# Optimization experiments

Measured on AMD Instinct MI355X. Metric: run time of the kernel, lower is better.

The kernel has to match this reference:

```python
import jax, jax.numpy as jnp
import numpy as np

H_DIM = 1024
HEAD_DIM = 128
N_HEADS = 8
HD = HEAD_DIM * N_HEADS  # 1024


def setup_inputs() -> dict:
    key = jax.random.key(0)
    ks = jax.random.split(key, 32)
    B, S = 16, 1024
    inp = {
        "f_in": jax.random.normal(ks[0], (B, S, H_DIM), jnp.float32),
        "i_in": jax.random.normal(ks[1], (B, S, H_DIM), jnp.float32),
        "z_in": jax.random.normal(ks[2], (B, S, H_DIM), jnp.float32),
        "o_in": jax.random.normal(ks[3], (B, S, H_DIM), jnp.float32),
        "c0": jax.random.normal(ks[4], (B, N_HEADS, HEAD_DIM), jnp.float32),
        "h0": jax.random.normal(ks[5], (B, N_HEADS, HEAD_DIM), jnp.float32),
    }
    # Parameters (torch Linear stored here as [in, out]; init std=0.02, zero bias)
    names_x = ["Fx", "Ix", "Zx", "Ox"]
    names_h = ["Fh", "Ih", "Zh", "Oh"]
    for j, n in enumerate(names_x):
        inp[f"W_{n}"] = 0.02 * jax.random.normal(ks[6 + j], (H_DIM, HD), jnp.float32)
        inp[f"b_{n}"] = jnp.zeros((HD,), jnp.float32)
    for j, n in enumerate(names_h):
        inp[f"W_{n}"] = 0.02 * jax.random.normal(ks[10 + j], (HD, HD), jnp.float32)
        inp[f"b_{n}"] = jnp.zeros((HD,), jnp.float32)
    inp["W_post"] = 0.02 * jax.random.normal(ks[14], (HD, H_DIM), jnp.float32)
    inp["b_post"] = jnp.zeros((H_DIM,), jnp.float32)
    return inp


def reference(f_in, i_in, z_in, o_in, c0, h0,
              W_Fx, b_Fx, W_Ix, b_Ix, W_Zx, b_Zx, W_Ox, b_Ox,
              W_Fh, b_Fh, W_Ih, b_Ih, W_Zh, b_Zh, W_Oh, b_Oh,
              W_post, b_post):
    B, S, _ = f_in.shape
    # Precompute input-to-gate projections for all timesteps: (B,S,HD)
    fx = f_in @ W_Fx + b_Fx
    ix = i_in @ W_Ix + b_Ix
    zx = z_in @ W_Zx + b_Zx
    ox = o_in @ W_Ox + b_Ox
    # Flatten head state: gating is elementwise, heads are contiguous in HD
    c = c0.reshape(B, HD)
    h = h0.reshape(B, HD)
    # Time-major for scan: (S,B,HD)
    xs = (fx.transpose(1, 0, 2), ix.transpose(1, 0, 2),
          zx.transpose(1, 0, 2), ox.transpose(1, 0, 2))

    def step(carry, x):
        c, h = carry
        fx_t, ix_t, zx_t, ox_t = x
        f = jax.nn.sigmoid(fx_t + h @ W_Fh + b_Fh)
        i = jax.nn.sigmoid(ix_t + h @ W_Ih + b_Ih)
        z = jnp.tanh(zx_t + h @ W_Zh + b_Zh)
        o = jax.nn.sigmoid(ox_t + h @ W_Oh + b_Oh)
        c = f * c + i * z
        h = o * jnp.tanh(c)
        return (c, h), h

    (c, h), ys = jax.lax.scan(step, (c, h), xs)
    y = ys.transpose(1, 0, 2)  # (B,S,HD)
    y = y @ W_post + b_post    # n_heads > 1 -> post-head projection
    state = (c.reshape(B, N_HEADS, HEAD_DIM), h.reshape(B, N_HEADS, HEAD_DIM))
    return (y, state)
```

## Files before the change

### kernel.cpp

```cpp
#include <hip/hip_runtime.h>
#include <stdint.h>
#include <stddef.h>

typedef __attribute__((ext_vector_type(8))) short short8;
typedef __attribute__((ext_vector_type(4))) short short4_t;
typedef __attribute__((ext_vector_type(8))) unsigned short ushort8_t;
typedef __attribute__((ext_vector_type(4))) unsigned short ushort4_t;
typedef __attribute__((ext_vector_type(4))) float f32x4;
typedef __attribute__((ext_vector_type(4))) unsigned uint4_t;
typedef __attribute__((ext_vector_type(2))) unsigned uint2_t;

#define XG_BYTES  (134217728ull)
#define HS_BYTES  (33587200ull)
#define PAD_OFF   (XG_BYTES + HS_BYTES)
#define WT_OFF    (PAD_OFF + 32768ull)

#define SENT 0x7FC07FC0u

__device__ __forceinline__ unsigned short f2b(float f){
  unsigned u = __builtin_bit_cast(unsigned, f);
  u += 0x7fffu + ((u >> 16) & 1u);
  return (unsigned short)(u >> 16);
}
__device__ __forceinline__ float b2f(unsigned short b){
  unsigned u = ((unsigned)b) << 16;
  return __builtin_bit_cast(float, u);
}
__device__ __forceinline__ float sigm(float x){ return 1.0f / (1.0f + __expf(-x)); }
__device__ __forceinline__ float tanh_(float x){ return 2.0f / (1.0f + __expf(-2.0f*x)) - 1.0f; }

__device__ __forceinline__ void ld_h8_plain(const unsigned short* p, short8* a){
  asm volatile(
    "global_load_dwordx4 %0, %8, off\n\t"
    "global_load_dwordx4 %1, %8, off offset:64\n\t"
    "global_load_dwordx4 %2, %8, off offset:128\n\t"
    "global_load_dwordx4 %3, %8, off offset:192\n\t"
    "global_load_dwordx4 %4, %8, off offset:256\n\t"
    "global_load_dwordx4 %5, %8, off offset:320\n\t"
    "global_load_dwordx4 %6, %8, off offset:384\n\t"
    "global_load_dwordx4 %7, %8, off offset:448\n\t"
    "s_waitcnt vmcnt(0)"
    : "=&v"(a[0]), "=&v"(a[1]), "=&v"(a[2]), "=&v"(a[3]),
      "=&v"(a[4]), "=&v"(a[5]), "=&v"(a[6]), "=&v"(a[7])
    : "v"(p) : "memory");
}
__device__ __forceinline__ void st_u32_mall(unsigned* p, unsigned v){
  asm volatile("global_store_dword %0, %1, off sc0 sc1"
               :: "v"(p), "v"(v) : "memory");
}

__global__ __launch_bounds__(256) void k_prep(
    const float* __restrict__ w0, const float* __restrict__ w1,
    const float* __restrict__ w2, const float* __restrict__ w3,
    const float* __restrict__ w4, const float* __restrict__ w5,
    const float* __restrict__ w6, const float* __restrict__ w7,
    const float* __restrict__ w8, unsigned short* __restrict__ wt)
{
  const int z = blockIdx.z;
  const float* W = (z==0)?w0:(z==1)?w1:(z==2)?w2:(z==3)?w3:(z==4)?w4:
                   (z==5)?w5:(z==6)?w6:(z==7)?w7:w8;
  unsigned short* out = wt + (size_t)z*1024*1024;
  __shared__ float tile[64][65];
  const int k0 = blockIdx.x*64, n0 = blockIdx.y*64;
  const int tid = threadIdx.x;
  {
    const int kk = tid >> 2, nn0 = (tid & 3) * 16;
    const float* src = W + (size_t)(k0+kk)*1024 + n0 + nn0;
    #pragma unroll
    for (int j=0;j<16;j+=4){
      f32x4 v = *(const f32x4*)(src + j);
      tile[kk][nn0+j+0]=v[0]; tile[kk][nn0+j+1]=v[1];
      tile[kk][nn0+j+2]=v[2]; tile[kk][nn0+j+3]=v[3];
    }
  }
  __syncthreads();
  {
    const int nn = tid >> 2, kk0 = (tid & 3) * 16;
    ushort8_t a, b;
    #pragma unroll
    for (int j=0;j<8;++j){ a[j]=f2b(tile[kk0+j][nn]); b[j]=f2b(tile[kk0+8+j][nn]); }
    unsigned short* dst = out + (size_t)(n0+nn)*1024 + k0 + kk0;
    *(ushort8_t*)dst = a;
    *(ushort8_t*)(dst+8) = b;
  }
}

__global__ void k_init(const float* __restrict__ h0, unsigned short* __restrict__ hs){
  const int i = blockIdx.x*256 + threadIdx.x;
  unsigned v = (unsigned)f2b(h0[i]);
  asm volatile("global_store_short %0, %1, off sc0 sc1"
               :: "v"(hs + i), "v"(v) : "memory");
}

__global__ void k_fill(unsigned* __restrict__ xgw, unsigned* __restrict__ hsw){
  const size_t i = (size_t)blockIdx.x*256 + threadIdx.x;
  uint4_t v = (uint4_t){SENT, SENT, SENT, SENT};
  if (i < 8388608ull){
    asm volatile("global_store_dwordx4 %0, %1, off sc0 sc1"
                 :: "v"(xgw + i*4), "v"(v) : "memory");
  } else {
    asm volatile("global_store_dwordx4 %0, %1, off sc0 sc1"
                 :: "v"(hsw + 8192 + (i - 8388608ull)*4), "v"(v) : "memory");
  }
}

__global__ __launch_bounds__(256,1) void k_mega(
    const float* __restrict__ xF, const float* __restrict__ xI,
    const float* __restrict__ xZ, const float* __restrict__ xO,
    const float* __restrict__ bF, const float* __restrict__ bI,
    const float* __restrict__ bZ, const float* __restrict__ bO,
    const unsigned short* __restrict__ wt,
    const float* __restrict__ bfh, const float* __restrict__ bih,
    const float* __restrict__ bzh, const float* __restrict__ boh,
    const float* __restrict__ c0,
    unsigned short* __restrict__ xg,
    unsigned short* __restrict__ hs,
    const float* __restrict__ bpost,
    float* __restrict__ y,
    float* __restrict__ oc, float* __restrict__ oh)
{
  __shared__ __align__(16) char smem[32768];
  const int tid  = threadIdx.x;
  const int lane = tid & 63, wv = tid >> 6;
  const int l15  = lane & 15, lg = lane >> 4;

  if (blockIdx.x < 64){
    typedef f32x4 PartT[4][4][64];
    PartT* part = (PartT*)smem;

    const unsigned short* WtR = wt + (size_t)5*1048576;
    const int wg = blockIdx.x;
    const int n  = wg*16 + l15;

    short8 wf[4][8];
    #pragma unroll
    for (int g=0; g<4; ++g){
      const unsigned short* wp = WtR + (size_t)g*1048576 + (size_t)n*1024 + wv*256 + lg*8;
      #pragma unroll
      for (int c=0; c<8; ++c)
        wf[g][c] = *(const short8*)(wp + c*32);
    }

    float cst[4]; float bias[4];
    bias[0]=bfh[n]; bias[1]=bih[n]; bias[2]=bzh[n]; bias[3]=boh[n];
    #pragma unroll
    for (int r=0;r<4;++r) cst[r] = c0[(size_t)(lg*4+r)*1024 + n];

    unsigned* hsw = (unsigned*)hs;
    const int koff = l15*1024 + wv*256 + lg*8;

    float hv = 0.f;
    for (int t=0; t<1024; ++t){
      short4_t xq[4];
      {
        const unsigned short* xb = xg + (size_t)((t*4)*1024 + n)*16 + lg*4;
        asm volatile(
          "global_load_dwordx2 %0, %4, off\n\t"
          "global_load_dwordx2 %1, %5, off\n\t"
          "global_load_dwordx2 %2, %6, off\n\t"
          "global_load_dwordx2 %3, %7, off"
          : "=&v"(xq[0]), "=&v"(xq[1]), "=&v"(xq[2]), "=&v"(xq[3])
          : "v"(xb), "v"(xb + 16384), "v"(xb + 32768), "v"(xb + 49152)
          : "memory");
      }

      const unsigned short* hp = hs + (size_t)t*16384 + koff;
      short8 a[8];
      ld_h8_plain(hp, a);
      {
        bool bad[8]; bool any = false;
        #pragma unroll
        for (int c=0;c<8;++c){
          uint4_t q = __builtin_bit_cast(uint4_t, a[c]);
          bad[c] = (q[0]==SENT)||(q[1]==SENT)||(q[2]==SENT)||(q[3]==SENT);
          any = any | bad[c];
        }
        while (__any(any)){
          __builtin_amdgcn_s_sleep(1);
          #pragma unroll
          for (int c=0;c<8;++c)
            if (bad[c])
              asm volatile("global_load_dwordx4 %0, %1, off sc0 sc1"
                           : "+v"(a[c]) : "v"(hp + c*32) : "memory");
          asm volatile("s_waitcnt vmcnt(0)" ::: "memory");
          __builtin_amdgcn_sched_barrier(0);
          any = false;
          #pragma unroll
          for (int c=0;c<8;++c){
            uint4_t q = __builtin_bit_cast(uint4_t, a[c]);
            bad[c] = (q[0]==SENT)||(q[1]==SENT)||(q[2]==SENT)||(q[3]==SENT);
            any = any | bad[c];
          }
        }
      }
      {
        bool xb_[4]; bool anyx = false;
        #pragma unroll
        for (int g=0; g<4; ++g){
          uint2_t u = __builtin_bit_cast(uint2_t, xq[g]);
          xb_[g] = (u[0]==SENT)||(u[1]==SENT);
          anyx = anyx | xb_[g];
        }
        while (__any(anyx)){
          __builtin_amdgcn_s_sleep(2);
          const unsigned short* xb = xg + (size_t)((t*4)*1024 + n)*16 + lg*4;
          #pragma unroll
          for (int g=0; g<4; ++g)
            if (xb_[g])
              asm volatile("global_load_dwordx2 %0, %1, off sc0 sc1"
                           : "+v"(xq[g]) : "v"(xb + g*16384) : "memory");
          asm volatile("s_waitcnt vmcnt(0)" ::: "memory");
          __builtin_amdgcn_sched_barrier(0);
          anyx = false;
          #pragma unroll
          for (int g=0; g<4; ++g){
            uint2_t u = __builtin_bit_cast(uint2_t, xq[g]);
            xb_[g] = (u[0]==SENT)||(u[1]==SENT);
            anyx = anyx | xb_[g];
          }
        }
      }

      f32x4 acc[4];
      #pragma unroll
      for (int g=0;g<4;++g) acc[g] = (f32x4){0.f,0.f,0.f,0.f};
      #pragma unroll
      for (int c=0;c<8;++c){
        acc[0] = __builtin_amdgcn_mfma_f32_16x16x32_bf16(a[c], wf[0][c], acc[0], 0,0,0);
        acc[1] = __builtin_amdgcn_mfma_f32_16x16x32_bf16(a[c], wf[1][c], acc[1], 0,0,0);
        acc[2] = __builtin_amdgcn_mfma_f32_16x16x32_bf16(a[c], wf[2][c], acc[2], 0,0,0);
        acc[3] = __builtin_amdgcn_mfma_f32_16x16x32_bf16(a[c], wf[3][c], acc[3], 0,0,0);
      }
      const int pb = t & 1;
      #pragma unroll
      for (int g=0;g<4;++g) part[pb][wv][g][lane] = acc[g];
      __syncthreads();

      f32x4 r_[4];
      #pragma unroll
      for (int g=0;g<4;++g){
        f32x4 s0 = part[pb][0][g][lane];
        f32x4 s1 = part[pb][1][g][lane];
        f32x4 s2 = part[pb][2][g][lane];
        f32x4 s3 = part[pb][3][g][lane];
        r_[g] = (s0 + s1) + (s2 + s3);
      }

      float hvv[4];
      {
        const int r = wv;
        float pf = r_[0][r] + b2f((unsigned short)xq[0][r]) + bias[0];
        float pi = r_[1][r] + b2f((unsigned short)xq[1][r]) + bias[1];
        float pz = r_[2][r] + b2f((unsigned short)xq[2][r]) + bias[2];
        float po = r_[3][r] + b2f((unsigned short)xq[3][r]) + bias[3];
        float fg = sigm(pf), ig = sigm(pi), zg = tanh_(pz), og = sigm(po);
        float cn = fg*cst[r] + ig*zg;
        cst[r] = cn;
        hv = og * tanh_(cn);
        hvv[r] = hv;
        unsigned m  = (unsigned)f2b(hv);
        unsigned nb = (unsigned)__shfl_xor(m, 1);
        if ((l15 & 1) == 0){
          unsigned word = m | (nb << 16);
          unsigned* pw = hsw + (size_t)(t+1)*8192 + (size_t)(lg*4+wv)*512 + (n >> 1);
          st_u32_mall(pw, word);
        }
      }
      #pragma unroll
      for (int r=0;r<4;++r){
        if (r == wv) continue;
        float pf = r_[0][r] + b2f((unsigned short)xq[0][r]) + bias[0];
        float pi = r_[1][r] + b2f((unsigned short)xq[1][r]) + bias[1];
        float pz = r_[2][r] + b2f((unsigned short)xq[2][r]) + bias[2];
        float po = r_[3][r] + b2f((unsigned short)xq[3][r]) + bias[3];
        float fg = sigm(pf), ig = sigm(pi), zg = tanh_(pz), og = sigm(po);
        float cn = fg*cst[r] + ig*zg;
        cst[r] = cn;
        hvv[r] = og * tanh_(cn);
      }
      if (t == 1023 && wv == 0){
        #pragma unroll
        for (int r=0;r<4;++r){
          oc[(size_t)(lg*4+r)*1024 + n] = cst[r];
          oh[(size_t)(lg*4+r)*1024 + n] = hvv[r];
        }
      }
    }
    return;
  }

  unsigned short* AsmB = (unsigned short*)smem;
  unsigned short* BsmB = (unsigned short*)(smem + 8192);
  const int wid = blockIdx.x - 64;
  const int wy = wv >> 1, wx = wv & 1;
  const int rr = tid >> 1, kq = tid & 1;
  const int s0 = kq*2;
  unsigned short* aw0 = &AsmB[rr*32 + (((s0  ) ^ (rr&3))<<3)];
  unsigned short* aw1 = &AsmB[rr*32 + (((s0+1) ^ (rr&3))<<3)];
  unsigned short* bw0 = &BsmB[rr*32 + (((s0  ) ^ (rr&3))<<3)];
  unsigned short* bw1 = &BsmB[rr*32 + (((s0+1) ^ (rr&3))<<3)];

  for (int idx = wid; idx < 4096; idx += 192){
    const int tm = idx >> 5, rmn = idx & 31, tn = rmn >> 2, g = rmn & 3;
    const float* X  = (g==0)?xF:(g==1)?xI:(g==2)?xZ:xO;
    const float* Bp = (g==0)?bF:(g==1)?bI:(g==2)?bZ:bO;
    const unsigned short* Wg = wt + (size_t)g*1048576;

    const int ar = tm*128 + rr;
    const int ab = ar & 15, as_ = ar >> 4;
    const float* aptr = X + ((size_t)ab*1024 + as_)*1024 + kq*16;
    const unsigned short* bp_ = Wg + (size_t)(tn*128 + rr)*1024 + kq*16;

    f32x4 acc[4][4];
    #pragma unroll
    for (int m=0;m<4;++m)
      #pragma unroll
      for (int q=0;q<4;++q) acc[m][q] = (f32x4){0.f,0.f,0.f,0.f};

    for (int k0=0; k0<1024; k0+=32){
      const float* ap = aptr + k0;
      f32x4 v0 = *(const f32x4*)(ap + 0);
      f32x4 v1 = *(const f32x4*)(ap + 4);
      f32x4 v2 = *(const f32x4*)(ap + 8);
      f32x4 v3 = *(const f32x4*)(ap + 12);
      ushort8_t pa, pb;
      #pragma unroll
      for (int j=0;j<4;++j){ pa[j]=f2b(v0[j]); pa[4+j]=f2b(v1[j]); pb[j]=f2b(v2[j]); pb[4+j]=f2b(v3[j]); }
      *(ushort8_t*)aw0 = pa;
      *(ushort8_t*)aw1 = pb;
      ushort8_t q0 = *(const ushort8_t*)(bp_ + k0);
      ushort8_t q1 = *(const ushort8_t*)(bp_ + k0 + 8);
      *(ushort8_t*)bw0 = q0;
      *(ushort8_t*)bw1 = q1;
      __syncthreads();

      short8 af[4], bf_[4];
      #pragma unroll
      for (int m=0;m<4;++m){
        int row = wy*64 + m*16 + l15;
        af[m] = *(const short8*)&AsmB[row*32 + ((lg ^ (row&3))<<3)];
      }
      #pragma unroll
      for (int q=0;q<4;++q){
        int row = wx*64 + q*16 + l15;
        bf_[q] = *(const short8*)&BsmB[row*32 + ((lg ^ (row&3))<<3)];
      }
      #pragma unroll
      for (int m=0;m<4;++m)
        #pragma unroll
        for (int q=0;q<4;++q)
          acc[m][q] = __builtin_amdgcn_mfma_f32_16x16x32_bf16(af[m], bf_[q], acc[m][q], 0,0,0);
      __syncthreads();
    }

    #pragma unroll
    for (int m=0;m<4;++m){
      const int t = tm*8 + wy*4 + m;
      #pragma unroll
      for (int q=0;q<4;++q){
        const int n = tn*128 + wx*64 + q*16 + l15;
        const float bias = Bp[n];
        f32x4 v = acc[m][q];
        ushort4_t pk;
        #pragma unroll
        for (int r=0;r<4;++r) pk[r] = f2b(v[r] + bias);
        uint2_t w2 = __builtin_bit_cast(uint2_t, pk);
        unsigned short* dst = xg + (size_t)((t*4+g)*1024 + n)*16 + lg*4;
        asm volatile("global_store_dwordx2 %0, %1, off sc0 sc1"
                     :: "v"(dst), "v"(w2) : "memory");
      }
    }
  }

  for (int idx = wid; idx < 1024; idx += 192){
    const int tm = idx >> 3, tn = idx & 7;
    const unsigned short* aptr = hs + 16384 + (size_t)(tm*128 + rr)*1024 + kq*16;
    const unsigned short* bp_  = wt + (size_t)4*1048576 + (size_t)(tn*128 + rr)*1024 + kq*16;

    f32x4 acc[4][4];
    #pragma unroll
    for (int m=0;m<4;++m)
      #pragma unroll
      for (int q=0;q<4;++q) acc[m][q] = (f32x4){0.f,0.f,0.f,0.f};

    for (int k0=0; k0<1024; k0+=32){
      ushort8_t a0, a1;
      asm volatile(
        "global_load_dwordx4 %0, %2, off\n\t"
        "global_load_dwordx4 %1, %3, off\n\t"
        "s_waitcnt vmcnt(0)"
        : "=&v"(a0), "=&v"(a1)
        : "v"(aptr + k0), "v"(aptr + k0 + 8) : "memory");
      __builtin_amdgcn_sched_barrier(0);
      {
        uint4_t q0 = __builtin_bit_cast(uint4_t, a0);
        uint4_t q1 = __builtin_bit_cast(uint4_t, a1);
        bool b0 = (q0[0]==SENT)||(q0[1]==SENT)||(q0[2]==SENT)||(q0[3]==SENT);
        bool b1 = (q1[0]==SENT)||(q1[1]==SENT)||(q1[2]==SENT)||(q1[3]==SENT);
        while (__any(b0 | b1)){
          __builtin_amdgcn_s_sleep(8);
          if (b0) asm volatile("global_load_dwordx4 %0, %1, off sc0 sc1"
                               : "+v"(a0) : "v"(aptr + k0) : "memory");
          if (b1) asm volatile("global_load_dwordx4 %0, %1, off sc0 sc1"
                               : "+v"(a1) : "v"(aptr + k0 + 8) : "memory");
          asm volatile("s_waitcnt vmcnt(0)" ::: "memory");
          __builtin_amdgcn_sched_barrier(0);
          q0 = __builtin_bit_cast(uint4_t, a0);
          q1 = __builtin_bit_cast(uint4_t, a1);
          b0 = (q0[0]==SENT)||(q0[1]==SENT)||(q0[2]==SENT)||(q0[3]==SENT);
          b1 = (q1[0]==SENT)||(q1[1]==SENT)||(q1[2]==SENT)||(q1[3]==SENT);
        }
      }
      *(ushort8_t*)aw0 = a0;
      *(ushort8_t*)aw1 = a1;
      ushort8_t q0v = *(const ushort8_t*)(bp_ + k0);
      ushort8_t q1v = *(const ushort8_t*)(bp_ + k0 + 8);
      *(ushort8_t*)bw0 = q0v;
      *(ushort8_t*)bw1 = q1v;
      __syncthreads();

      short8 af[4], bf_[4];
      #pragma unroll
      for (int m=0;m<4;++m){
        int row = wy*64 + m*16 + l15;
        af[m] = *(const short8*)&AsmB[row*32 + ((lg ^ (row&3))<<3)];
      }
      #pragma unroll
      for (int q=0;q<4;++q){
        int row = wx*64 + q*16 + l15;
        bf_[q] = *(const short8*)&BsmB[row*32 + ((lg ^ (row&3))<<3)];
      }
      #pragma unroll
      for (int m=0;m<4;++m)
        #pragma unroll
        for (int q=0;q<4;++q)
          acc[m][q] = __builtin_amdgcn_mfma_f32_16x16x32_bf16(af[m], bf_[q], acc[m][q], 0,0,0);
      __syncthreads();
    }

    #pragma unroll
    for (int m=0;m<4;++m){
      const int s = tm*8 + wy*4 + m;
      #pragma unroll
      for (int q=0;q<4;++q){
        const int n = tn*128 + wx*64 + q*16 + l15;
        const float bias = bpost[n];
        f32x4 v = acc[m][q];
        #pragma unroll
        for (int r=0;r<4;++r){
          const int b = lg*4 + r;
          y[((size_t)b << 20) + ((size_t)s << 10) + n] = v[r] + bias;
        }
      }
    }
  }
}

extern "C" void kernel_launch(void* const* d_in, const int* in_sizes, int n_in,
                              void* d_out, int out_size, void* d_ws, size_t ws_size,
                              hipStream_t stream)
{
  const float* f_in = (const float*)d_in[0];
  const float* i_in = (const float*)d_in[1];
  const float* z_in = (const float*)d_in[2];
  const float* o_in = (const float*)d_in[3];
  const float* c0   = (const float*)d_in[4];
  const float* h0   = (const float*)d_in[5];
  const float* W_Fx = (const float*)d_in[6];  const float* b_Fx = (const float*)d_in[7];
  const float* W_Ix = (const float*)d_in[8];  const float* b_Ix = (const float*)d_in[9];
  const float* W_Zx = (const float*)d_in[10]; const float* b_Zx = (const float*)d_in[11];
  const float* W_Ox = (const float*)d_in[12]; const float* b_Ox = (const float*)d_in[13];
  const float* W_Fh = (const float*)d_in[14]; const float* b_Fh = (const float*)d_in[15];
  const float* W_Ih = (const float*)d_in[16]; const float* b_Ih = (const float*)d_in[17];
  const float* W_Zh = (const float*)d_in[18]; const float* b_Zh = (const float*)d_in[19];
  const float* W_Oh = (const float*)d_in[20]; const float* b_Oh = (const float*)d_in[21];
  const float* W_post = (const float*)d_in[22]; const float* b_post = (const float*)d_in[23];

  char* ws = (char*)d_ws;
  unsigned short* xg = (unsigned short*)(ws);
  unsigned short* hs = (unsigned short*)(ws + XG_BYTES);
  unsigned short* wt = (unsigned short*)(ws + WT_OFF);

  float* y  = (float*)d_out;
  float* oc = y + 16777216;
  float* oh = oc + 16384;

  k_prep<<<dim3(16,16,9), 256, 0, stream>>>(W_Fx, W_Ix, W_Zx, W_Ox, W_post,
                                            W_Fh, W_Ih, W_Zh, W_Oh, wt);
  k_init<<<64, 256, 0, stream>>>(h0, hs);
  k_fill<<<40960, 256, 0, stream>>>((unsigned*)xg, (unsigned*)hs);
  k_mega<<<256, 256, 0, stream>>>(f_in, i_in, z_in, o_in,
                                  b_Fx, b_Ix, b_Zx, b_Ox,
                                  wt,
                                  b_Fh, b_Ih, b_Zh, b_Oh,
                                  c0, xg, hs, b_post, y, oc, oh);
}
```

Measured before the change: 3.556 ms.

## Give each recurrent wave the full K range to drop the LDS reduction barrier

Before, the four waves of each recurrent block split K four ways and reduced their partial sums through shared memory behind a __syncthreads every timestep. Now each wave computes its four output columns for all four gates over the full K=1024, with the gate index packed into the lane's N position. Gate values are regrouped with cross-lane shuffles, so no barrier or LDS round-trip is needed. In exchange each wave loads 4x more h data per step (32 dwordx4 loads), holds 32 weight fragments in registers, and every lane recomputes the gate math redundantly.

```diff
diff --git a/kernel.cpp b/kernel.cpp
--- a/kernel.cpp
+++ b/kernel.cpp
@@ -29,21 +29,19 @@
 __device__ __forceinline__ float sigm(float x){ return 1.0f / (1.0f + __expf(-x)); }
 __device__ __forceinline__ float tanh_(float x){ return 2.0f / (1.0f + __expf(-2.0f*x)) - 1.0f; }
 
-__device__ __forceinline__ void ld_h8_plain(const unsigned short* p, short8* a){
-  asm volatile(
-    "global_load_dwordx4 %0, %8, off\n\t"
-    "global_load_dwordx4 %1, %8, off offset:64\n\t"
-    "global_load_dwordx4 %2, %8, off offset:128\n\t"
-    "global_load_dwordx4 %3, %8, off offset:192\n\t"
-    "global_load_dwordx4 %4, %8, off offset:256\n\t"
-    "global_load_dwordx4 %5, %8, off offset:320\n\t"
-    "global_load_dwordx4 %6, %8, off offset:384\n\t"
-    "global_load_dwordx4 %7, %8, off offset:448\n\t"
-    "s_waitcnt vmcnt(0)"
-    : "=&v"(a[0]), "=&v"(a[1]), "=&v"(a[2]), "=&v"(a[3]),
-      "=&v"(a[4]), "=&v"(a[5]), "=&v"(a[6]), "=&v"(a[7])
-    : "v"(p) : "memory");
-}
+#define ISSUE8P(p, A) asm volatile( \
+    "global_load_dwordx4 %0, %8, off\n\t" \
+    "global_load_dwordx4 %1, %8, off offset:64\n\t" \
+    "global_load_dwordx4 %2, %8, off offset:128\n\t" \
+    "global_load_dwordx4 %3, %8, off offset:192\n\t" \
+    "global_load_dwordx4 %4, %8, off offset:256\n\t" \
+    "global_load_dwordx4 %5, %8, off offset:320\n\t" \
+    "global_load_dwordx4 %6, %8, off offset:384\n\t" \
+    "global_load_dwordx4 %7, %8, off offset:448" \
+    : "=&v"((A)[0]), "=&v"((A)[1]), "=&v"((A)[2]), "=&v"((A)[3]), \
+      "=&v"((A)[4]), "=&v"((A)[5]), "=&v"((A)[6]), "=&v"((A)[7]) \
+    : "v"(p) : "memory")
+
 __device__ __forceinline__ void st_u32_mall(unsigned* p, unsigned v){
   asm volatile("global_store_dword %0, %1, off sc0 sc1"
                :: "v"(p), "v"(v) : "memory");
@@ -125,35 +123,33 @@
   const int l15  = lane & 15, lg = lane >> 4;
 
   if (blockIdx.x < 64){
-    typedef f32x4 PartT[4][4][64];
-    PartT* part = (PartT*)smem;
-
     const unsigned short* WtR = wt + (size_t)5*1048576;
-    const int wg = blockIdx.x;
-    const int n  = wg*16 + l15;
-
-    short8 wf[4][8];
-    #pragma unroll
-    for (int g=0; g<4; ++g){
-      const unsigned short* wp = WtR + (size_t)g*1048576 + (size_t)n*1024 + wv*256 + lg*8;
-      #pragma unroll
-      for (int c=0; c<8; ++c)
-        wf[g][c] = *(const short8*)(wp + c*32);
-    }
-
-    float cst[4]; float bias[4];
-    bias[0]=bfh[n]; bias[1]=bih[n]; bias[2]=bzh[n]; bias[3]=boh[n];
-    #pragma unroll
-    for (int r=0;r<4;++r) cst[r] = c0[(size_t)(lg*4+r)*1024 + n];
+    const int wg  = blockIdx.x;
+    const int n0  = wg*16 + wv*4;
+    const int g_  = l15 >> 2;
+    const int c_  = l15 & 3;
+    const int col = n0 + c_;
+
+    short8 wf[32];
+    {
+      const unsigned short* wp = WtR + (size_t)g_*1048576 + (size_t)col*1024 + lg*8;
+      #pragma unroll
+      for (int ch=0; ch<32; ++ch)
+        wf[ch] = *(const short8*)(wp + ch*32);
+    }
+
+    float cst[4];
+    #pragma unroll
+    for (int r=0;r<4;++r) cst[r] = c0[(size_t)(lg*4+r)*1024 + col];
+    const float bias_[4] = {bfh[col], bih[col], bzh[col], boh[col]};
 
     unsigned* hsw = (unsigned*)hs;
-    const int koff = l15*1024 + wv*256 + lg*8;
-
-    float hv = 0.f;
+    float hvout[4] = {0.f,0.f,0.f,0.f};
+
     for (int t=0; t<1024; ++t){
       short4_t xq[4];
       {
-        const unsigned short* xb = xg + (size_t)((t*4)*1024 + n)*16 + lg*4;
+        const unsigned short* xb = xg + (size_t)((t*4)*1024 + col)*16 + lg*4;
         asm volatile(
           "global_load_dwordx2 %0, %4, off\n\t"
           "global_load_dwordx2 %1, %5, off\n\t"
@@ -164,126 +160,124 @@
           : "memory");
       }
 
-      const unsigned short* hp = hs + (size_t)t*16384 + koff;
-      short8 a[8];
-      ld_h8_plain(hp, a);
+      const unsigned short* hp = hs + (size_t)t*16384 + (size_t)l15*1024 + lg*8;
+      short8 a[32];
+      ISSUE8P(hp,        a);
+      ISSUE8P(hp +  256, a + 8);
+      ISSUE8P(hp +  512, a + 16);
+      ISSUE8P(hp +  768, a + 24);
+      asm volatile("s_waitcnt vmcnt(0)" ::: "memory");
+      __builtin_amdgcn_sched_barrier(0);
+
       {
-        bool bad[8]; bool any = false;
-        #pragma unroll
-        for (int c=0;c<8;++c){
-          uint4_t q = __builtin_bit_cast(uint4_t, a[c]);
-          bad[c] = (q[0]==SENT)||(q[1]==SENT)||(q[2]==SENT)||(q[3]==SENT);
-          any = any | bad[c];
+        bool bad[32]; bool any = false;
+        #pragma unroll
+        for (int ch=0; ch<32; ++ch){
+          uint4_t q = __builtin_bit_cast(uint4_t, a[ch]);
+          bad[ch] = (q[0]==SENT)||(q[1]==SENT)||(q[2]==SENT)||(q[3]==SENT);
+          any = any | bad[ch];
         }
         while (__any(any)){
           __builtin_amdgcn_s_sleep(1);
           #pragma unroll
-          for (int c=0;c<8;++c)
-            if (bad[c])
+          for (int ch=0; ch<32; ++ch)
+            if (bad[ch])
               asm volatile("global_load_dwordx4 %0, %1, off sc0 sc1"
-                           : "+v"(a[c]) : "v"(hp + c*32) : "memory");
+                           : "+v"(a[ch]) : "v"(hp + ch*32) : "memory");
           asm volatile("s_waitcnt vmcnt(0)" ::: "memory");
           __builtin_amdgcn_sched_barrier(0);
           any = false;
           #pragma unroll
-          for (int c=0;c<8;++c){
-            uint4_t q = __builtin_bit_cast(uint4_t, a[c]);
-            bad[c] = (q[0]==SENT)||(q[1]==SENT)||(q[2]==SENT)||(q[3]==SENT);
-            any = any | bad[c];
+          for (int ch=0; ch<32; ++ch){
+            uint4_t q = __builtin_bit_cast(uint4_t, a[ch]);
+            bad[ch] = (q[0]==SENT)||(q[1]==SENT)||(q[2]==SENT)||(q[3]==SENT);
+            any = any | bad[ch];
           }
         }
       }
       {
         bool xb_[4]; bool anyx = false;
         #pragma unroll
-        for (int g=0; g<4; ++g){
-          uint2_t u = __builtin_bit_cast(uint2_t, xq[g]);
-          xb_[g] = (u[0]==SENT)||(u[1]==SENT);
-          anyx = anyx | xb_[g];
+        for (int m=0; m<4; ++m){
+          uint2_t u = __builtin_bit_cast(uint2_t, xq[m]);
+          xb_[m] = (u[0]==SENT)||(u[1]==SENT);
+          anyx = anyx | xb_[m];
         }
         while (__any(anyx)){
           __builtin_amdgcn_s_sleep(2);
-          const unsigned short* xb = xg + (size_t)((t*4)*1024 + n)*16 + lg*4;
+          const unsigned short* xb = xg + (size_t)((t*4)*1024 + col)*16 + lg*4;
           #pragma unroll
-          for (int g=0; g<4; ++g)
-            if (xb_[g])
+          for (int m=0; m<4; ++m)
+            if (xb_[m])
               asm volatile("global_load_dwordx2 %0, %1, off sc0 sc1"
-                           : "+v"(xq[g]) : "v"(xb + g*16384) : "memory");
+                           : "+v"(xq[m]) : "v"(xb + m*16384) : "memory");
           asm volatile("s_waitcnt vmcnt(0)" ::: "memory");
           __builtin_amdgcn_sched_barrier(0);
           anyx = false;
           #pragma unroll
-          for (int g=0; g<4; ++g){
-            uint2_t u = __builtin_bit_cast(uint2_t, xq[g]);
-            xb_[g] = (u[0]==SENT)||(u[1]==SENT);
-            anyx = anyx | xb_[g];
+          for (int m=0; m<4; ++m){
+            uint2_t u = __builtin_bit_cast(uint2_t, xq[m]);
+            xb_[m] = (u[0]==SENT)||(u[1]==SENT);
+            anyx = anyx | xb_[m];
           }
         }
       }
 
-      f32x4 acc[4];
-      #pragma unroll
-      for (int g=0;g<4;++g) acc[g] = (f32x4){0.f,0.f,0.f,0.f};
-      #pragma unroll
-      for (int c=0;c<8;++c){
-        acc[0] = __builtin_amdgcn_mfma_f32_16x16x32_bf16(a[c], wf[0][c], acc[0], 0,0,0);
-        acc[1] = __builtin_amdgcn_mfma_f32_16x16x32_bf16(a[c], wf[1][c], acc[1], 0,0,0);
-        acc[2] = __builtin_amdgcn_mfma_f32_16x16x32_bf16(a[c], wf[2][c], acc[2], 0,0,0);
-        acc[3] = __builtin_amdgcn_mfma_f32_16x16x32_bf16(a[c], wf[3][c], acc[3], 0,0,0);
-      }
-      const int pb = t & 1;
-      #pragma unroll
-      for (int g=0;g<4;++g) part[pb][wv][g][lane] = acc[g];
-      __syncthreads();
-
-      f32x4 r_[4];
-      #pragma unroll
-      for (int g=0;g<4;++g){
-        f32x4 s0 = part[pb][0][g][lane];
-        f32x4 s1 = part[pb][1][g][lane];
-        f32x4 s2 = part[pb][2][g][lane];
-        f32x4 s3 = part[pb][3][g][lane];
-        r_[g] = (s0 + s1) + (s2 + s3);
-      }
-
-      float hvv[4];
-      {
-        const int r = wv;
-        float pf = r_[0][r] + b2f((unsigned short)xq[0][r]) + bias[0];
-        float pi = r_[1][r] + b2f((unsigned short)xq[1][r]) + bias[1];
-        float pz = r_[2][r] + b2f((unsigned short)xq[2][r]) + bias[2];
-        float po = r_[3][r] + b2f((unsigned short)xq[3][r]) + bias[3];
+      f32x4 ac0 = (f32x4){0,0,0,0}, ac1 = (f32x4){0,0,0,0};
+      f32x4 ac2 = (f32x4){0,0,0,0}, ac3 = (f32x4){0,0,0,0};
+      #pragma unroll
+      for (int ch=0; ch<32; ch+=4){
+        ac0 = __builtin_amdgcn_mfma_f32_16x16x32_bf16(a[ch+0], wf[ch+0], ac0, 0,0,0);
+        ac1 = __builtin_amdgcn_mfma_f32_16x16x32_bf16(a[ch+1], wf[ch+1], ac1, 0,0,0);
+        ac2 = __builtin_amdgcn_mfma_f32_16x16x32_bf16(a[ch+2], wf[ch+2], ac2, 0,0,0);
+        ac3 = __builtin_amdgcn_mfma_f32_16x16x32_bf16(a[ch+3], wf[ch+3], ac3, 0,0,0);
+      }
+      f32x4 accv = (ac0 + ac1) + (ac2 + ac3);
+
+      f32x4 vB, vC, vD;
+      #pragma unroll
+      for (int r=0;r<4;++r){
+        vB[r] = __shfl_xor(accv[r], 4);
+        vC[r] = __shfl_xor(accv[r], 8);
+        vD[r] = __shfl_xor(vB[r],   8);
+      }
+      f32x4 rg[4];
+      #pragma unroll
+      for (int m=0;m<4;++m){
+        const int s = g_ ^ m;
+        rg[m] = (s==0) ? accv : (s==1) ? vB : (s==2) ? vC : vD;
+      }
+
+      #pragma unroll
+      for (int r=0;r<4;++r){
+        const int sh = r*16;
+        float pf = rg[0][r] + b2f((unsigned short)(__builtin_bit_cast(unsigned long long, xq[0]) >> sh)) + bias_[0];
+        float pi = rg[1][r] + b2f((unsigned short)(__builtin_bit_cast(unsigned long long, xq[1]) >> sh)) + bias_[1];
+        float pz = rg[2][r] + b2f((unsigned short)(__builtin_bit_cast(unsigned long long, xq[2]) >> sh)) + bias_[2];
+        float po = rg[3][r] + b2f((unsigned short)(__builtin_bit_cast(unsigned long long, xq[3]) >> sh)) + bias_[3];
         float fg = sigm(pf), ig = sigm(pi), zg = tanh_(pz), og = sigm(po);
         float cn = fg*cst[r] + ig*zg;
         cst[r] = cn;
-        hv = og * tanh_(cn);
-        hvv[r] = hv;
-        unsigned m  = (unsigned)f2b(hv);
+        hvout[r] = og * tanh_(cn);
+      }
+
+      #pragma unroll
+      for (int r=0;r<4;++r){
+        unsigned m  = (unsigned)f2b(hvout[r]);
         unsigned nb = (unsigned)__shfl_xor(m, 1);
-        if ((l15 & 1) == 0){
+        if (g_ == 0 && (c_ & 1) == 0){
           unsigned word = m | (nb << 16);
-          unsigned* pw = hsw + (size_t)(t+1)*8192 + (size_t)(lg*4+wv)*512 + (n >> 1);
+          unsigned* pw = hsw + (size_t)(t+1)*8192 + (size_t)(lg*4+r)*512 + (col >> 1);
           st_u32_mall(pw, word);
         }
       }
+    }
+
+    if (g_ == 0){
       #pragma unroll
       for (int r=0;r<4;++r){
-        if (r == wv) continue;
-        float pf = r_[0][r] + b2f((unsigned short)xq[0][r]) + bias[0];
-        float pi = r_[1][r] + b2f((unsigned short)xq[1][r]) + bias[1];
-        float pz = r_[2][r] + b2f((unsigned short)xq[2][r]) + bias[2];
-        float po = r_[3][r] + b2f((unsigned short)xq[3][r]) + bias[3];
-        float fg = sigm(pf), ig = sigm(pi), zg = tanh_(pz), og = sigm(po);
-        float cn = fg*cst[r] + ig*zg;
-        cst[r] = cn;
-        hvv[r] = og * tanh_(cn);
-      }
-      if (t == 1023 && wv == 0){
-        #pragma unroll
-        for (int r=0;r<4;++r){
-          oc[(size_t)(lg*4+r)*1024 + n] = cst[r];
-          oh[(size_t)(lg*4+r)*1024 + n] = hvv[r];
-        }
+        oc[(size_t)(lg*4+r)*1024 + col] = cst[r];
+        oh[(size_t)(lg*4+r)*1024 + col] = hvout[r];
       }
     }
     return;
```

Measured after the change: 12.82 ms. 261% more time.
